# Kernel tuning notes

Hardware: AMD Instinct MI355X
Metric: run time of the kernel (lower is better)

Reference implementation:

```python
import jax, jax.numpy as jnp
import numpy as np

N = 131072      # H*W*batch = 128*128*8 features
D = 256         # feature_dim
P = 64          # proj_dim
E = 260096      # (2*H*W - H - W)*batch edges of the grid graph
G = 8192        # number of groups
SIM_THRESHOLD = 0.5


def setup_inputs() -> dict:
    key = jax.random.key(0)
    k0, k1, k2, k3 = jax.random.split(key, 4)
    features = jax.random.normal(k0, (N, D), dtype=jnp.float32)
    proj_W = jax.random.normal(k1, (D, P), dtype=jnp.float32) / np.sqrt(D)
    edge_index = jax.random.randint(k2, (2, E), 0, N, dtype=jnp.int64)
    group_ids = jax.random.randint(k3, (N,), 0, G, dtype=jnp.int64)
    return {
        "features": features,
        "proj_W": proj_W,
        "edge_index": edge_index,
        "group_ids": group_ids,
        "num_groups": G,
    }


def reference(features, proj_W, edge_index, group_ids, num_groups):
    # Projection: [N, D] @ [D, P] -> [N, P]
    proj = features @ proj_W
    # Pair comparison: gather both endpoints per edge, dot product per edge
    src, dst = edge_index[0], edge_index[1]
    sims = jnp.sum(proj[src] * proj[dst], axis=-1)            # [E]
    edge_logits = jax.nn.sigmoid(sims - SIM_THRESHOLD)        # [E]
    # Group mean pooling: scatter-add features per group, divide by size
    ones = jnp.ones((features.shape[0],), dtype=features.dtype)
    group_sums = jax.ops.segment_sum(features, group_ids, num_segments=num_groups)  # [G, D]
    group_sizes = jax.ops.segment_sum(ones, group_ids, num_segments=num_groups)     # [G]
    group_sizes = jnp.maximum(group_sizes, 1.0)
    group_means = group_sums / group_sizes[:, None]           # [G, D]
    return group_means, edge_logits
```

## Files before the change

### kernel.cpp

```cpp
#include <hip/hip_runtime.h>
#include <math.h>

constexpr int Nn = 131072;
constexpr int Dd = 256;
constexpr int Pp = 64;
constexpr int Gg = 8192;
constexpr int Ee = 260096;
constexpr float SIM_TH = 0.5f;

typedef _Float16 half8 __attribute__((ext_vector_type(8)));
typedef float floatx4 __attribute__((ext_vector_type(4)));

__global__ __launch_bounds__(256) void k_count_wfrag(
    const int* __restrict__ gid, int* __restrict__ cnt,
    const float* __restrict__ W, _Float16* __restrict__ Wf)
{
    const int i = blockIdx.x * 256 + threadIdx.x;
    atomicAdd(&cnt[gid[i]], 1);
    if (i < 16384) {
        const int j = i & 7;
        const int l = (i >> 3) & 63;
        const int t = (i >> 9) & 3;
        const int c = i >> 11;
        const int k = c * 32 + (l >> 4) * 8 + j;
        const int n = t * 16 + (l & 15);
        Wf[i] = (_Float16)W[k * Pp + n];
    }
}

__global__ __launch_bounds__(256) void k_scan(
    const int* __restrict__ cnt,
    int* __restrict__ offsets,
    int* __restrict__ cursor)
{
    __shared__ int lds[256];
    const int t = threadIdx.x;
    const int base = t * 32;

    int s = 0;
#pragma unroll
    for (int j = 0; j < 32; ++j) s += cnt[base + j];
    lds[t] = s;
    __syncthreads();

    int v = s;
    for (int off = 1; off < 256; off <<= 1) {
        int add = (t >= off) ? lds[t - off] : 0;
        __syncthreads();
        v += add;
        lds[t] = v;
        __syncthreads();
    }

    int run = v - s;
    for (int j = 0; j < 32; ++j) {
        offsets[base + j] = run;
        cursor[base + j]  = run;
        run += cnt[base + j];
    }
}

__global__ __launch_bounds__(256) void k_mid(
    const float* __restrict__ A,
    const _Float16* __restrict__ Wf,
    _Float16* __restrict__ proj,
    const int* __restrict__ gid,
    int* __restrict__ cursor,
    int* __restrict__ bucket)
{
    if (blockIdx.x < 512) {
        const int i = blockIdx.x * 256 + threadIdx.x;
        const int p = atomicAdd(&cursor[gid[i]], 1);
        bucket[p] = i;
        return;
    }

    __shared__ _Float16 WfL[16384];
    {
        const int t = threadIdx.x;
        const float4* __restrict__ src = reinterpret_cast<const float4*>(Wf);
        float4* dst = reinterpret_cast<float4*>(WfL);
#pragma unroll
        for (int q = 0; q < 8; ++q)
            dst[t + 256 * q] = src[t + 256 * q];
    }
    __syncthreads();

    const int blk = blockIdx.x - 512;
    const int l = threadIdx.x & 63;
    const int w = threadIdx.x >> 6;
    const int rowbase = blk * 64 + w * 16;
    const int am = l & 15;
    const int q  = l >> 4;

    const float* __restrict__ arow = A + (size_t)(rowbase + am) * Dd + q * 8;
    const half8* __restrict__ bfrag = reinterpret_cast<const half8*>(WfL) + l;

    floatx4 acc[4];
#pragma unroll
    for (int t = 0; t < 4; ++t) acc[t] = (floatx4){0.f, 0.f, 0.f, 0.f};

#pragma unroll
    for (int c = 0; c < 8; ++c) {
        const float4 fa = *reinterpret_cast<const float4*>(arow + c * 32);
        const float4 fb = *reinterpret_cast<const float4*>(arow + c * 32 + 4);
        half8 a;
        a[0] = (_Float16)fa.x; a[1] = (_Float16)fa.y;
        a[2] = (_Float16)fa.z; a[3] = (_Float16)fa.w;
        a[4] = (_Float16)fb.x; a[5] = (_Float16)fb.y;
        a[6] = (_Float16)fb.z; a[7] = (_Float16)fb.w;
        const half8 b0 = bfrag[(c * 4 + 0) * 64];
        const half8 b1 = bfrag[(c * 4 + 1) * 64];
        const half8 b2 = bfrag[(c * 4 + 2) * 64];
        const half8 b3 = bfrag[(c * 4 + 3) * 64];
        acc[0] = __builtin_amdgcn_mfma_f32_16x16x32_f16(a, b0, acc[0], 0, 0, 0);
        acc[1] = __builtin_amdgcn_mfma_f32_16x16x32_f16(a, b1, acc[1], 0, 0, 0);
        acc[2] = __builtin_amdgcn_mfma_f32_16x16x32_f16(a, b2, acc[2], 0, 0, 0);
        acc[3] = __builtin_amdgcn_mfma_f32_16x16x32_f16(a, b3, acc[3], 0, 0, 0);
    }

#pragma unroll
    for (int t = 0; t < 4; ++t) {
#pragma unroll
        for (int r = 0; r < 4; ++r) {
            proj[(size_t)(rowbase + q * 4 + r) * Pp + t * 16 + am] =
                (_Float16)acc[t][r];
        }
    }
}

__global__ __launch_bounds__(256) void k_tail(
    const float* __restrict__ features,
    const int* __restrict__ bucket,
    const int* __restrict__ offsets,
    const int* __restrict__ cnt,
    float* __restrict__ out_means,
    const _Float16* __restrict__ proj,
    const int* __restrict__ ei,
    float* __restrict__ out_logits)
{
    if (blockIdx.x < 2048) {
        const int lane = threadIdx.x & 63;
        const int g = blockIdx.x * 4 + (threadIdx.x >> 6);
        const int n = cnt[g];
        const int start = offsets[g];
        const int col = lane * 4;
        const int* __restrict__ bk = bucket + start;

        float4 s = make_float4(0.f, 0.f, 0.f, 0.f);
        int k = 0;
        for (; k + 16 <= n; k += 16) {
            int r[16];
#pragma unroll
            for (int u = 0; u < 16; ++u) r[u] = bk[k + u];
            float4 f[16];
#pragma unroll
            for (int u = 0; u < 16; ++u)
                f[u] = *reinterpret_cast<const float4*>(features + (size_t)r[u] * Dd + col);
#pragma unroll
            for (int u = 0; u < 16; ++u) {
                s.x += f[u].x; s.y += f[u].y; s.z += f[u].z; s.w += f[u].w;
            }
        }
        for (; k + 4 <= n; k += 4) {
            int r[4];
#pragma unroll
            for (int u = 0; u < 4; ++u) r[u] = bk[k + u];
            float4 f[4];
#pragma unroll
            for (int u = 0; u < 4; ++u)
                f[u] = *reinterpret_cast<const float4*>(features + (size_t)r[u] * Dd + col);
#pragma unroll
            for (int u = 0; u < 4; ++u) {
                s.x += f[u].x; s.y += f[u].y; s.z += f[u].z; s.w += f[u].w;
            }
        }
        for (; k < n; ++k) {
            const float4 f = *reinterpret_cast<const float4*>(features + (size_t)bk[k] * Dd + col);
            s.x += f.x; s.y += f.y; s.z += f.z; s.w += f.w;
        }
        const float inv = 1.0f / (float)max(n, 1);
        s.x *= inv; s.y *= inv; s.z *= inv; s.w *= inv;
        *reinterpret_cast<float4*>(out_means + (size_t)g * Dd + col) = s;
        return;
    }

    const int bid = blockIdx.x - 2048;
    const int sub = threadIdx.x & 7;
    const int sg  = bid * 32 + (threadIdx.x >> 3);
    const int e0  = sg * 4;

    int s[4], t[4];
#pragma unroll
    for (int u = 0; u < 4; ++u) { s[u] = ei[e0 + u]; t[u] = ei[Ee + e0 + u]; }

    half8 a[4], b[4];
#pragma unroll
    for (int u = 0; u < 4; ++u) {
        a[u] = *reinterpret_cast<const half8*>(proj + (size_t)s[u] * Pp + sub * 8);
        b[u] = *reinterpret_cast<const half8*>(proj + (size_t)t[u] * Pp + sub * 8);
    }

    float v[4];
#pragma unroll
    for (int u = 0; u < 4; ++u) {
        float acc = 0.f;
#pragma unroll
        for (int j = 0; j < 8; ++j)
            acc = fmaf((float)a[u][j], (float)b[u][j], acc);
        v[u] = acc;
    }

#pragma unroll
    for (int off = 4; off >= 1; off >>= 1) {
#pragma unroll
        for (int u = 0; u < 4; ++u) v[u] += __shfl_xor(v[u], off, 64);
    }

    if (sub < 4) {
        const float x = v[sub];
        out_logits[e0 + sub] = 1.0f / (1.0f + __expf(-(x - SIM_TH)));
    }
}

extern "C" void kernel_launch(void* const* d_in, const int* in_sizes, int n_in,
                              void* d_out, int out_size, void* d_ws, size_t ws_size,
                              hipStream_t stream)
{
    const float* features = (const float*)d_in[0];
    const float* W        = (const float*)d_in[1];
    const int*   ei       = (const int*)d_in[2];
    const int*   gid      = (const int*)d_in[3];

    float* out_means  = (float*)d_out;
    float* out_logits = out_means + (size_t)Gg * Dd;

    _Float16*  proj    = (_Float16*)d_ws;
    int*       bucket  = (int*)(proj + (size_t)Nn * Pp);
    int*       cnt     = bucket + Nn;
    int*       offsets = cnt + Gg;
    int*       cursor  = offsets + Gg;
    _Float16*  Wf      = (_Float16*)(cursor + Gg);

    hipMemsetAsync(cnt, 0, (size_t)Gg * sizeof(int), stream);

    hipLaunchKernelGGL(k_count_wfrag, dim3(Nn / 256), dim3(256), 0, stream,
                       gid, cnt, W, Wf);
    hipLaunchKernelGGL(k_scan, dim3(1), dim3(256), 0, stream,
                       cnt, offsets, cursor);
    hipLaunchKernelGGL(k_mid, dim3(512 + Nn / 64), dim3(256), 0, stream,
                       features, Wf, proj, gid, cursor, bucket);
    hipLaunchKernelGGL(k_tail, dim3(2048 + Ee / 128), dim3(256), 0, stream,
                       features, bucket, offsets, cnt, out_means,
                       proj, ei, out_logits);
}
```

Baseline: 248.0 us.

## Regroup stages so the scan overlaps the projection GEMM and bucketing overlaps edge scoring

Kernel boundaries are rearranged. The single-block prefix scan now runs as block 0 of the projection GEMM kernel. Bucket filling runs alongside the edge-logit computation, and group-mean pooling becomes its own final kernel. The GEMM also reads the W fragments straight from global memory instead of staging them in LDS. The intent is to hide the serial one-block scan and balance the work across launches, while the launch count stays at four, with the risk that uncached global B-fragment reads slow the GEMM.

```diff
diff --git a/kernel.cpp b/kernel.cpp
--- a/kernel.cpp
+++ b/kernel.cpp
@@ -11,7 +11,7 @@
 typedef _Float16 half8 __attribute__((ext_vector_type(8)));
 typedef float floatx4 __attribute__((ext_vector_type(4)));
 
-__global__ __launch_bounds__(256) void k_count_wfrag(
+__global__ __launch_bounds__(256) void k_a(
     const int* __restrict__ gid, int* __restrict__ cnt,
     const float* __restrict__ W, _Float16* __restrict__ Wf)
 {
@@ -28,65 +28,44 @@
     }
 }
 
-__global__ __launch_bounds__(256) void k_scan(
+__global__ __launch_bounds__(256) void k_b(
+    const float* __restrict__ A,
+    const _Float16* __restrict__ Wf,
+    _Float16* __restrict__ proj,
     const int* __restrict__ cnt,
     int* __restrict__ offsets,
     int* __restrict__ cursor)
 {
-    __shared__ int lds[256];
-    const int t = threadIdx.x;
-    const int base = t * 32;
-
-    int s = 0;
-#pragma unroll
-    for (int j = 0; j < 32; ++j) s += cnt[base + j];
-    lds[t] = s;
-    __syncthreads();
-
-    int v = s;
-    for (int off = 1; off < 256; off <<= 1) {
-        int add = (t >= off) ? lds[t - off] : 0;
+    if (blockIdx.x == 0) {
+        __shared__ int lds[256];
+        const int t = threadIdx.x;
+        const int base = t * 32;
+
+        int s = 0;
+#pragma unroll
+        for (int j = 0; j < 32; ++j) s += cnt[base + j];
+        lds[t] = s;
         __syncthreads();
-        v += add;
-        lds[t] = v;
-        __syncthreads();
-    }
-
-    int run = v - s;
-    for (int j = 0; j < 32; ++j) {
-        offsets[base + j] = run;
-        cursor[base + j]  = run;
-        run += cnt[base + j];
-    }
-}
-
-__global__ __launch_bounds__(256) void k_mid(
-    const float* __restrict__ A,
-    const _Float16* __restrict__ Wf,
-    _Float16* __restrict__ proj,
-    const int* __restrict__ gid,
-    int* __restrict__ cursor,
-    int* __restrict__ bucket)
-{
-    if (blockIdx.x < 512) {
-        const int i = blockIdx.x * 256 + threadIdx.x;
-        const int p = atomicAdd(&cursor[gid[i]], 1);
-        bucket[p] = i;
+
+        int v = s;
+        for (int off = 1; off < 256; off <<= 1) {
+            int add = (t >= off) ? lds[t - off] : 0;
+            __syncthreads();
+            v += add;
+            lds[t] = v;
+            __syncthreads();
+        }
+
+        int run = v - s;
+        for (int j = 0; j < 32; ++j) {
+            offsets[base + j] = run;
+            cursor[base + j]  = run;
+            run += cnt[base + j];
+        }
         return;
     }
 
-    __shared__ _Float16 WfL[16384];
-    {
-        const int t = threadIdx.x;
-        const float4* __restrict__ src = reinterpret_cast<const float4*>(Wf);
-        float4* dst = reinterpret_cast<float4*>(WfL);
-#pragma unroll
-        for (int q = 0; q < 8; ++q)
-            dst[t + 256 * q] = src[t + 256 * q];
-    }
-    __syncthreads();
-
-    const int blk = blockIdx.x - 512;
+    const int blk = blockIdx.x - 1;
     const int l = threadIdx.x & 63;
     const int w = threadIdx.x >> 6;
     const int rowbase = blk * 64 + w * 16;
@@ -94,7 +73,7 @@
     const int q  = l >> 4;
 
     const float* __restrict__ arow = A + (size_t)(rowbase + am) * Dd + q * 8;
-    const half8* __restrict__ bfrag = reinterpret_cast<const half8*>(WfL) + l;
+    const half8* __restrict__ bfrag = reinterpret_cast<const half8*>(Wf) + l;
 
     floatx4 acc[4];
 #pragma unroll
@@ -129,98 +108,108 @@
     }
 }
 
-__global__ __launch_bounds__(256) void k_tail(
+__global__ __launch_bounds__(256) void k_c(
+    const int* __restrict__ gid,
+    int* __restrict__ cursor,
+    int* __restrict__ bucket,
+    const _Float16* __restrict__ proj,
+    const int* __restrict__ ei,
+    float* __restrict__ out_logits)
+{
+    if (blockIdx.x < 512) {
+        const int i = blockIdx.x * 256 + threadIdx.x;
+        const int p = atomicAdd(&cursor[gid[i]], 1);
+        bucket[p] = i;
+        return;
+    }
+
+    const int bid = blockIdx.x - 512;
+    const int sub = threadIdx.x & 7;
+    const int sg  = bid * 32 + (threadIdx.x >> 3);
+    const int e0  = sg * 4;
+
+    int s[4], t[4];
+#pragma unroll
+    for (int u = 0; u < 4; ++u) { s[u] = ei[e0 + u]; t[u] = ei[Ee + e0 + u]; }
+
+    half8 a[4], b[4];
+#pragma unroll
+    for (int u = 0; u < 4; ++u) {
+        a[u] = *reinterpret_cast<const half8*>(proj + (size_t)s[u] * Pp + sub * 8);
+        b[u] = *reinterpret_cast<const half8*>(proj + (size_t)t[u] * Pp + sub * 8);
+    }
+
+    float v[4];
+#pragma unroll
+    for (int u = 0; u < 4; ++u) {
+        float acc = 0.f;
+#pragma unroll
+        for (int j = 0; j < 8; ++j)
+            acc = fmaf((float)a[u][j], (float)b[u][j], acc);
+        v[u] = acc;
+    }
+
+#pragma unroll
+    for (int off = 4; off >= 1; off >>= 1) {
+#pragma unroll
+        for (int u = 0; u < 4; ++u) v[u] += __shfl_xor(v[u], off, 64);
+    }
+
+    if (sub < 4) {
+        const float x = v[sub];
+        out_logits[e0 + sub] = 1.0f / (1.0f + __expf(-(x - SIM_TH)));
+    }
+}
+
+__global__ __launch_bounds__(256) void k_d(
     const float* __restrict__ features,
     const int* __restrict__ bucket,
     const int* __restrict__ offsets,
     const int* __restrict__ cnt,
-    float* __restrict__ out_means,
-    const _Float16* __restrict__ proj,
-    const int* __restrict__ ei,
-    float* __restrict__ out_logits)
-{
-    if (blockIdx.x < 2048) {
-        const int lane = threadIdx.x & 63;
-        const int g = blockIdx.x * 4 + (threadIdx.x >> 6);
-        const int n = cnt[g];
-        const int start = offsets[g];
-        const int col = lane * 4;
-        const int* __restrict__ bk = bucket + start;
-
-        float4 s = make_float4(0.f, 0.f, 0.f, 0.f);
-        int k = 0;
-        for (; k + 16 <= n; k += 16) {
-            int r[16];
-#pragma unroll
-            for (int u = 0; u < 16; ++u) r[u] = bk[k + u];
-            float4 f[16];
-#pragma unroll
-            for (int u = 0; u < 16; ++u)
-                f[u] = *reinterpret_cast<const float4*>(features + (size_t)r[u] * Dd + col);
-#pragma unroll
-            for (int u = 0; u < 16; ++u) {
-                s.x += f[u].x; s.y += f[u].y; s.z += f[u].z; s.w += f[u].w;
-            }
-        }
-        for (; k + 4 <= n; k += 4) {
-            int r[4];
-#pragma unroll
-            for (int u = 0; u < 4; ++u) r[u] = bk[k + u];
-            float4 f[4];
-#pragma unroll
-            for (int u = 0; u < 4; ++u)
-                f[u] = *reinterpret_cast<const float4*>(features + (size_t)r[u] * Dd + col);
-#pragma unroll
-            for (int u = 0; u < 4; ++u) {
-                s.x += f[u].x; s.y += f[u].y; s.z += f[u].z; s.w += f[u].w;
-            }
-        }
-        for (; k < n; ++k) {
-            const float4 f = *reinterpret_cast<const float4*>(features + (size_t)bk[k] * Dd + col);
-            s.x += f.x; s.y += f.y; s.z += f.z; s.w += f.w;
-        }
-        const float inv = 1.0f / (float)max(n, 1);
-        s.x *= inv; s.y *= inv; s.z *= inv; s.w *= inv;
-        *reinterpret_cast<float4*>(out_means + (size_t)g * Dd + col) = s;
-        return;
-    }
-
-    const int bid = blockIdx.x - 2048;
-    const int sub = threadIdx.x & 7;
-    const int sg  = bid * 32 + (threadIdx.x >> 3);
-    const int e0  = sg * 4;
-
-    int s[4], t[4];
-#pragma unroll
-    for (int u = 0; u < 4; ++u) { s[u] = ei[e0 + u]; t[u] = ei[Ee + e0 + u]; }
-
-    half8 a[4], b[4];
-#pragma unroll
-    for (int u = 0; u < 4; ++u) {
-        a[u] = *reinterpret_cast<const half8*>(proj + (size_t)s[u] * Pp + sub * 8);
-        b[u] = *reinterpret_cast<const half8*>(proj + (size_t)t[u] * Pp + sub * 8);
-    }
-
-    float v[4];
-#pragma unroll
-    for (int u = 0; u < 4; ++u) {
-        float acc = 0.f;
-#pragma unroll
-        for (int j = 0; j < 8; ++j)
-            acc = fmaf((float)a[u][j], (float)b[u][j], acc);
-        v[u] = acc;
-    }
-
-#pragma unroll
-    for (int off = 4; off >= 1; off >>= 1) {
-#pragma unroll
-        for (int u = 0; u < 4; ++u) v[u] += __shfl_xor(v[u], off, 64);
-    }
-
-    if (sub < 4) {
-        const float x = v[sub];
-        out_logits[e0 + sub] = 1.0f / (1.0f + __expf(-(x - SIM_TH)));
-    }
+    float* __restrict__ out_means)
+{
+    const int lane = threadIdx.x & 63;
+    const int g = blockIdx.x * 4 + (threadIdx.x >> 6);
+    const int n = cnt[g];
+    const int start = offsets[g];
+    const int col = lane * 4;
+    const int* __restrict__ bk = bucket + start;
+
+    float4 s = make_float4(0.f, 0.f, 0.f, 0.f);
+    int k = 0;
+    for (; k + 16 <= n; k += 16) {
+        int r[16];
+#pragma unroll
+        for (int u = 0; u < 16; ++u) r[u] = bk[k + u];
+        float4 f[16];
+#pragma unroll
+        for (int u = 0; u < 16; ++u)
+            f[u] = *reinterpret_cast<const float4*>(features + (size_t)r[u] * Dd + col);
+#pragma unroll
+        for (int u = 0; u < 16; ++u) {
+            s.x += f[u].x; s.y += f[u].y; s.z += f[u].z; s.w += f[u].w;
+        }
+    }
+    for (; k + 4 <= n; k += 4) {
+        int r[4];
+#pragma unroll
+        for (int u = 0; u < 4; ++u) r[u] = bk[k + u];
+        float4 f[4];
+#pragma unroll
+        for (int u = 0; u < 4; ++u)
+            f[u] = *reinterpret_cast<const float4*>(features + (size_t)r[u] * Dd + col);
+#pragma unroll
+        for (int u = 0; u < 4; ++u) {
+            s.x += f[u].x; s.y += f[u].y; s.z += f[u].z; s.w += f[u].w;
+        }
+    }
+    for (; k < n; ++k) {
+        const float4 f = *reinterpret_cast<const float4*>(features + (size_t)bk[k] * Dd + col);
+        s.x += f.x; s.y += f.y; s.z += f.z; s.w += f.w;
+    }
+    const float inv = 1.0f / (float)max(n, 1);
+    s.x *= inv; s.y *= inv; s.z *= inv; s.w *= inv;
+    *reinterpret_cast<float4*>(out_means + (size_t)g * Dd + col) = s;
 }
 
 extern "C" void kernel_launch(void* const* d_in, const int* in_sizes, int n_in,
@@ -244,13 +233,12 @@
 
     hipMemsetAsync(cnt, 0, (size_t)Gg * sizeof(int), stream);
 
-    hipLaunchKernelGGL(k_count_wfrag, dim3(Nn / 256), dim3(256), 0, stream,
+    hipLaunchKernelGGL(k_a, dim3(Nn / 256), dim3(256), 0, stream,
                        gid, cnt, W, Wf);
-    hipLaunchKernelGGL(k_scan, dim3(1), dim3(256), 0, stream,
-                       cnt, offsets, cursor);
-    hipLaunchKernelGGL(k_mid, dim3(512 + Nn / 64), dim3(256), 0, stream,
-                       features, Wf, proj, gid, cursor, bucket);
-    hipLaunchKernelGGL(k_tail, dim3(2048 + Ee / 128), dim3(256), 0, stream,
-                       features, bucket, offsets, cnt, out_means,
-                       proj, ei, out_logits);
-}
+    hipLaunchKernelGGL(k_b, dim3(1 + Nn / 64), dim3(256), 0, stream,
+                       features, Wf, proj, cnt, offsets, cursor);
+    hipLaunchKernelGGL(k_c, dim3(512 + Ee / 128), dim3(256), 0, stream,
+                       gid, cursor, bucket, proj, ei, out_logits);
+    hipLaunchKernelGGL(k_d, dim3(Gg / 4), dim3(256), 0, stream,
+                       features, bucket, offsets, cnt, out_means);
+}
```

After: 248.6 us. Within noise of the previous version (+0.2%).
